# Optimization experiments

Hardware: AMD Instinct MI355X
Metric: run time of the kernel (lower is better)

Reference implementation:

```python
import jax, jax.numpy as jnp
import numpy as np

N_CLASS, N_SUPPORT, N_QUERY = 5, 5, 15
C, T, V = 128, 8, 25
LN_EPS = 1e-12


def setup_inputs() -> dict:
    key = jax.random.key(0)
    ks = jax.random.split(key, 6)
    n_tot = N_CLASS * (N_SUPPORT + N_QUERY)
    inp = jax.random.normal(ks[0], (n_tot, C, T, V), dtype=jnp.float32)
    # episode labels: 20 consecutive samples per class (arange // per_class)
    target = (jnp.arange(n_tot, dtype=jnp.int32) // (N_SUPPORT + N_QUERY)).astype(jnp.int32)
    s = 0.02
    p = lambda k: jax.random.normal(k, (C, C), dtype=jnp.float32) * s
    return {
        'input': inp,
        'Wq': p(ks[1]), 'bq': jnp.zeros((C,), jnp.float32),
        'Wk': p(ks[2]), 'bk': jnp.zeros((C,), jnp.float32),
        'Wv': p(ks[3]), 'bv': jnp.zeros((C,), jnp.float32),
        'Wo': p(ks[4]), 'bo': jnp.zeros((C,), jnp.float32),
        'ln_g': jnp.ones((C,), jnp.float32), 'ln_b': jnp.zeros((C,), jnp.float32),
        'target': target,
        'n_support': N_SUPPORT,
    }


def _layer_norm(x, g, b):
    mu = x.mean(-1, keepdims=True)
    var = ((x - mu) ** 2).mean(-1, keepdims=True)
    return (x - mu) * jax.lax.rsqrt(var + LN_EPS) * g + b


def _episode_forward(input, Wq, bq, Wk, bk, Wv, bv, Wo, bo, ln_g, ln_b, target, n_support):
    n_tot, c, t, v = input.shape
    m = N_CLASS
    per_class = n_tot // m
    n_query = per_class - n_support
    n = m * n_query

    # support/query split (stable argsort == torch.where per class for sorted labels)
    order = jnp.argsort(target).reshape(m, per_class)
    supp_idx = order[:, :n_support]                      # (m, h)
    qry_idx = order[:, n_support:].reshape(-1)           # (n,)
    z_proto = input[supp_idx]                            # (m, h, c, t, v)
    zq = input[qry_idx]                                  # (n, c, t, v)

    # ---- hal(): pairwise cross-attention over the vertex axis ----
    mh = m * n_support
    zq_p = jnp.transpose(zq, (0, 2, 3, 1))                                   # (n, t, v, c)
    zp_p = jnp.transpose(z_proto.reshape(mh, c, t, v), (0, 2, 3, 1))          # (mh, t, v, c)
    cat = jnp.concatenate([zq_p, zp_p], axis=0)                               # (n1, t, v, c)
    n1 = cat.shape[0]

    # Q from each of the n1 items, K/V from each of the mh prototypes.
    # Equivalent to the original expand->reshape pairing, without duplicating K/V.
    Q = cat @ Wq + bq                                                         # (n1, t, v, c)
    K = zp_p @ Wk + bk                                                        # (mh, t, v, c)
    Vv = zp_p @ Wv + bv                                                       # (mh, t, v, c)
    scale = 1.0 / jnp.sqrt(jnp.asarray(c, dtype=Q.dtype))
    scores = jnp.einsum('ntqc,mtkc->nmtqk', Q, K) * scale                     # (n1, mh, t, v, v)
    attn = jax.nn.softmax(scores, axis=-1)
    ctx = jnp.einsum('nmtqk,mtkc->nmtqc', attn, Vv)                           # (n1, mh, t, v, c)
    out = _layer_norm(ctx @ Wo + bo + cat[:, None], ln_g, ln_b)               # residual + LN
    att = out.mean(axis=1)                                                    # (n1, t, v, c) mean over mh pairs

    zq_att = jnp.transpose(att[:n], (0, 3, 1, 2))                             # (n, c, t, v)
    proto_att = att[n:].reshape(m, n_support, t, v, c).mean(axis=1)           # (m, t, v, c)
    proto_att = jnp.transpose(proto_att, (0, 3, 1, 2))                        # (m, c, t, v)

    # ---- squared-Euclidean metric on flattened features ----
    zq_f = zq_att.reshape(n, -1)
    zp_f = proto_att.reshape(m, -1)
    dist = jnp.sum((zq_f[:, None, :] - zp_f[None, :, :]) ** 2, axis=-1)       # (n, m)

    log_p_y = jax.nn.log_softmax(-dist, axis=1).reshape(m, n_query, m)
    cls = jnp.arange(m)
    loss = -log_p_y[cls[:, None], jnp.arange(n_query)[None, :], cls[:, None]].mean()
    y_hat = jnp.argmax(log_p_y, axis=2)
    acc = (y_hat == cls[:, None]).astype(jnp.float32).mean()
    return loss, acc


def reference(input, Wq, bq, Wk, bk, Wv, bv, Wo, bo, ln_g, ln_b, target, n_support):
    return _episode_forward(input, Wq, bq, Wk, bk, Wv, bv, Wo, bo, ln_g, ln_b, target, n_support)
```

## Files before the change

### kernel.cpp

```cpp
#include <hip/hip_runtime.h>
#include <math.h>

#define NTOT 100
#define NQ   75
#define NP   25
#define CC   128
#define TT   8
#define VV   25
#define NCLS 5
#define NSUP 5
#define NQRY 15
#define ROW  (TT*VV*CC)
#define TILE (VV*CC)
#define ROWS_Q 20000
#define ROWS_S 5000
#define RB_Q 625
#define RB_S 157

typedef __attribute__((ext_vector_type(8))) short short8;
typedef __attribute__((ext_vector_type(16))) float f32x16;

typedef union { uint4 u4; short8 s8; } pk_t;

__device__ __forceinline__ ushort f2bf(float f) {
    uint u = __float_as_uint(f);
    u += 0x7FFFu + ((u >> 16) & 1u);
    return (ushort)(u >> 16);
}
__device__ __forceinline__ float bf2f(uint u16v) {
    return __uint_as_float(u16v << 16);
}
__device__ __forceinline__ uint pkbf(float a, float b) {
    return (uint)f2bf(a) | ((uint)f2bf(b) << 16);
}

__global__ __launch_bounds__(256) void k_proj(
    const float* __restrict__ input, const int* __restrict__ target,
    const float* __restrict__ Wq, const float* __restrict__ Wk,
    const float* __restrict__ Wv, const float* __restrict__ Wo,
    const float* __restrict__ bq, const float* __restrict__ bk,
    const float* __restrict__ bv,
    ushort* __restrict__ catC, ushort* __restrict__ Qf,
    ushort* __restrict__ Kf, ushort* __restrict__ Vf,
    int* __restrict__ counter) {
    __shared__ ushort WfragLDS[16384];
    __shared__ ushort VtFrag[16384];

    int b = blockIdx.x, tid = threadIdx.x;
    int w = tid >> 6, lane = tid & 63, half = lane >> 5, l31 = lane & 31;

    if (b == 0 && tid == 0) *counter = 0;

    int* iscr = (int*)VtFrag;
    if (tid < NTOT) iscr[tid] = target[tid];
    __syncthreads();
    if (tid < NTOT) {
        int ti = iscr[tid], rank = 0;
        for (int j = 0; j < NTOT; ++j) {
            int tj = iscr[j];
            rank += (tj < ti) || (tj == ti && j < tid);
        }
        iscr[128 + rank] = tid;
    }
    __syncthreads();

    bool isQ = b < 157;
    int rowblk = isQ ? (b * 4 + w) : ((b - 157) * 4 + w);
    int nrb = isQ ? RB_Q : RB_S;
    bool act = rowblk < nrb;
    int rlimit = isQ ? ROWS_Q : ROWS_S;
    int grow = rowblk * 32 + l31;
    int growc = grow < rlimit ? grow : rlimit - 1;
    int n = growc / 200;
    int tv = growc - n * 200;
    int src;
    {
        int nn = isQ ? n : (NQ + n);
        if (nn < NQ) { int m = nn / NQRY, qq = nn - m * NQRY; src = iscr[128 + m * 20 + NSUP + qq]; }
        else         { int i2 = nn - NQ; int m = i2 / NSUP, s = i2 - m * NSUP; src = iscr[128 + m * 20 + s]; }
    }
    __syncthreads();

    const float* inp = input + (size_t)src * ROW + tv;
    short8 af[8];
    #pragma unroll
    for (int ks = 0; ks < 8; ++ks) {
        float f0 = inp[(ks * 16 + half * 8 + 0) * 200];
        float f1 = inp[(ks * 16 + half * 8 + 1) * 200];
        float f2 = inp[(ks * 16 + half * 8 + 2) * 200];
        float f3 = inp[(ks * 16 + half * 8 + 3) * 200];
        float f4 = inp[(ks * 16 + half * 8 + 4) * 200];
        float f5 = inp[(ks * 16 + half * 8 + 5) * 200];
        float f6 = inp[(ks * 16 + half * 8 + 6) * 200];
        float f7 = inp[(ks * 16 + half * 8 + 7) * 200];
        pk_t u;
        u.u4 = make_uint4(pkbf(f0, f1), pkbf(f2, f3), pkbf(f4, f5), pkbf(f6, f7));
        af[ks] = u.s8;
    }

    #define BUILDW(W) do {                                                       \
        for (int o = tid; o < 2048; o += 256) {                                  \
            int k8 = o >> 7, c = o & 127;                                        \
            uint4 pk;                                                            \
            pk.x = pkbf((W)[(k8*8+0)*128 + c], (W)[(k8*8+1)*128 + c]);           \
            pk.y = pkbf((W)[(k8*8+2)*128 + c], (W)[(k8*8+3)*128 + c]);           \
            pk.z = pkbf((W)[(k8*8+4)*128 + c], (W)[(k8*8+5)*128 + c]);           \
            pk.w = pkbf((W)[(k8*8+6)*128 + c], (W)[(k8*8+7)*128 + c]);           \
            int dst = (((c >> 5) * 8 + (k8 >> 1)) * 64 + ((c & 31) + 32 * (k8 & 1))) * 8; \
            *(uint4*)(WfragLDS + dst) = pk;                                      \
        }                                                                        \
    } while (0)

    if (isQ) {
        BUILDW(Wq);
        __syncthreads();
        #pragma unroll
        for (int ct = 0; ct < 4; ++ct) {
            if (!act) continue;
            f32x16 Cm;
            #pragma unroll
            for (int r = 0; r < 16; ++r) Cm[r] = 0.f;
            const ushort* bp = WfragLDS + ct * 8 * 512 + lane * 8;
            #pragma unroll
            for (int ks = 0; ks < 8; ++ks) {
                short8 bf_ = *(const short8*)(bp + ks * 512);
                Cm = __builtin_amdgcn_mfma_f32_32x32x16_bf16(af[ks], bf_, Cm, 0, 0, 0);
            }
            float bcol = bq[ct * 32 + l31];
            #pragma unroll
            for (int r = 0; r < 16; ++r) {
                int row = rowblk * 32 + (r & 3) + 8 * (r >> 2) + 4 * half;
                if (row < ROWS_Q) {
                    int c = ct * 32 + l31;
                    int st = row / 25, vv = row - st * 25;
                    size_t dst = (((size_t)st * 8 + (c >> 4)) * 64 + (vv + 32 * ((c >> 3) & 1))) * 8 + (c & 7);
                    Qf[dst] = f2bf(Cm[r] + bcol);
                }
            }
        }
        if (act) {
            ushort* cc = catC + (size_t)grow * 128 + half * 8;
            #pragma unroll
            for (int ks = 0; ks < 8; ++ks)
                *(short8*)(cc + ks * 16) = af[ks];
        }
    } else {
        BUILDW(Wk);
        __syncthreads();
        #pragma unroll
        for (int ct = 0; ct < 4; ++ct) {
            if (!act) continue;
            f32x16 Cm;
            #pragma unroll
            for (int r = 0; r < 16; ++r) Cm[r] = 0.f;
            const ushort* bp = WfragLDS + ct * 8 * 512 + lane * 8;
            #pragma unroll
            for (int ks = 0; ks < 8; ++ks) {
                short8 bf_ = *(const short8*)(bp + ks * 512);
                Cm = __builtin_amdgcn_mfma_f32_32x32x16_bf16(af[ks], bf_, Cm, 0, 0, 0);
            }
            float bcol = bk[ct * 32 + l31];
            #pragma unroll
            for (int r = 0; r < 16; ++r) {
                int row = rowblk * 32 + (r & 3) + 8 * (r >> 2) + 4 * half;
                if (row < ROWS_S) {
                    int c = ct * 32 + l31;
                    int st = row / 25, vv = row - st * 25;
                    size_t dst = (((size_t)st * 8 + (c >> 4)) * 64 + (vv + 32 * ((c >> 3) & 1))) * 8 + (c & 7);
                    Kf[dst] = f2bf(Cm[r] + bcol);
                }
            }
        }
        __syncthreads();
        BUILDW(Wv);
        __syncthreads();
        #pragma unroll
        for (int ct = 0; ct < 4; ++ct) {
            if (!act) continue;
            f32x16 Cm;
            #pragma unroll
            for (int r = 0; r < 16; ++r) Cm[r] = 0.f;
            const ushort* bp = WfragLDS + ct * 8 * 512 + lane * 8;
            #pragma unroll
            for (int ks = 0; ks < 8; ++ks) {
                short8 bf_ = *(const short8*)(bp + ks * 512);
                Cm = __builtin_amdgcn_mfma_f32_32x32x16_bf16(af[ks], bf_, Cm, 0, 0, 0);
            }
            float bcol = bv[ct * 32 + l31];
            int c = ct * 32 + l31;
            int ks2 = c >> 4, lh = (c >> 3) & 1, j2 = c & 7;
            #pragma unroll
            for (int r = 0; r < 16; ++r) {
                int rowLocal = (r & 3) + 8 * (r >> 2) + 4 * half;
                VtFrag[w * 4096 + ks2 * 512 + (rowLocal + 32 * lh) * 8 + j2] = f2bf(Cm[r] + bcol);
            }
        }
        __syncthreads();
        BUILDW(Wo);
        __syncthreads();
        short8 a2[8];
        if (act) {
            #pragma unroll
            for (int ks = 0; ks < 8; ++ks)
                a2[ks] = *(const short8*)(VtFrag + w * 4096 + ks * 512 + lane * 8);
        }
        #pragma unroll
        for (int ct = 0; ct < 4; ++ct) {
            if (!act) continue;
            f32x16 Cm;
            #pragma unroll
            for (int r = 0; r < 16; ++r) Cm[r] = 0.f;
            const ushort* bp = WfragLDS + ct * 8 * 512 + lane * 8;
            #pragma unroll
            for (int ks = 0; ks < 8; ++ks) {
                short8 bf_ = *(const short8*)(bp + ks * 512);
                Cm = __builtin_amdgcn_mfma_f32_32x32x16_bf16(a2[ks], bf_, Cm, 0, 0, 0);
            }
            #pragma unroll
            for (int r = 0; r < 16; ++r) {
                int row = rowblk * 32 + (r & 3) + 8 * (r >> 2) + 4 * half;
                if (row < ROWS_S) {
                    int c = ct * 32 + l31;
                    int tile = row / 25, vv = row - tile * 25;
                    size_t dst = ((((size_t)tile * 4 + ct) * 2 + (vv >> 4)) * 64
                                  + ((c & 31) + 32 * ((vv & 15) >> 3))) * 8 + (vv & 7);
                    Vf[dst] = f2bf(Cm[r]);
                }
            }
        }
    }
    #undef BUILDW
}

__global__ __launch_bounds__(256, 2) void k_attn(
    const ushort* __restrict__ Qf, const ushort* __restrict__ Kf,
    const ushort* __restrict__ Vf, const ushort* __restrict__ catC,
    const float* __restrict__ bo, float* __restrict__ att) {
    __shared__ float catb[25 * 129];
    __shared__ float red[2][50][65];
    __shared__ ushort qls[4096];

    int pair = blockIdx.x;
    int t = pair & 7;
    int tid = threadIdx.x;
    int wv = tid >> 6, lane = tid & 63;
    int q = lane & 31, half = lane >> 5;

    {
        const uint* cc = (const uint*)catC + (size_t)pair * 1600;
        for (int i2 = tid; i2 < 1600; i2 += 256) {
            uint u = cc[i2];
            int r = i2 >> 6, c2 = (i2 & 63) * 2;
            catb[r * 129 + c2]     = bf2f(u & 0xffffu) + bo[c2];
            catb[r * 129 + c2 + 1] = bf2f(u >> 16) + bo[c2 + 1];
        }
    }
    {
        const uint* qp = (const uint*)(Qf + (size_t)pair * 4096);
        uint* ql = (uint*)qls;
        for (int i2 = tid; i2 < 2048; i2 += 256) ql[i2] = qp[i2];
    }
    __syncthreads();

    int qc = q < 25 ? q : 24;
    float attsum[64];
    #pragma unroll
    for (int i = 0; i < 64; ++i) attsum[i] = 0.f;
    float Csc = 0.f;

    const float CEXP = (float)(1.4426950408889634 * 0.08838834764831845);

    const ushort* kbase = Kf + (size_t)t * 4096 + lane * 8;
    short8 kf[8];
    #pragma unroll
    for (int ks = 0; ks < 8; ++ks)
        kf[ks] = *(const short8*)(kbase + (size_t)wv * 32768 + ks * 512);

    int cnt = (wv == 0) ? 7 : 6;
    for (int mi = 0; mi < cnt; ++mi) {
        int m = wv + 4 * mi;

        f32x16 S;
        #pragma unroll
        for (int r = 0; r < 16; ++r) S[r] = 0.f;
        #pragma unroll
        for (int ks = 0; ks < 8; ++ks) {
            short8 qv = *(const short8*)(qls + ks * 512 + lane * 8);
            S = __builtin_amdgcn_mfma_f32_32x32x16_bf16(kf[ks], qv, S, 0, 0, 0);
        }

        float p[16], mx = -3e38f;
        #pragma unroll
        for (int r = 0; r < 16; ++r) {
            int key = (r & 3) + 8 * (r >> 2) + 4 * half;
            float v = (key < 25) ? S[r] : -3e38f;
            p[r] = v; mx = fmaxf(mx, v);
        }
        mx = fmaxf(mx, __shfl_xor(mx, 32));
        float sum = 0.f;
        #pragma unroll
        for (int r = 0; r < 16; ++r) { p[r] = exp2f((p[r] - mx) * CEXP); sum += p[r]; }
        sum += __shfl_xor(sum, 32);
        float inv = 1.f / sum;

        const ushort* vp = Vf + ((size_t)(m * 8 + t)) * 4096 + lane * 8;
        short8 vf0 = *(const short8*)(vp);
        short8 vf1 = *(const short8*)(vp + 512);
        short8 vf2 = *(const short8*)(vp + 1024);
        short8 vf3 = *(const short8*)(vp + 1536);
        short8 vf4 = *(const short8*)(vp + 2048);
        short8 vf5 = *(const short8*)(vp + 2560);
        short8 vf6 = *(const short8*)(vp + 3072);
        short8 vf7 = *(const short8*)(vp + 3584);
        #pragma unroll
        for (int ks = 0; ks < 8; ++ks)
            kf[ks] = *(const short8*)(kbase + (size_t)(m + 4) * 32768 + ks * 512);

        uint o01   = pkbf(p[0] * inv,  p[1] * inv);
        uint o23   = pkbf(p[2] * inv,  p[3] * inv);
        uint o45   = pkbf(p[4] * inv,  p[5] * inv);
        uint o67   = pkbf(p[6] * inv,  p[7] * inv);
        uint o89   = pkbf(p[8] * inv,  p[9] * inv);
        uint o1011 = pkbf(p[10] * inv, p[11] * inv);
        uint o1213 = pkbf(p[12] * inv, p[13] * inv);
        uint o1415 = pkbf(p[14] * inv, p[15] * inv);
        bool h0 = (half == 0);
        uint rA = __shfl_xor(h0 ? o45 : o01, 32);
        uint rB = __shfl_xor(h0 ? o67 : o23, 32);
        uint rC = __shfl_xor(h0 ? o1213 : o89, 32);
        uint rD = __shfl_xor(h0 ? o1415 : o1011, 32);
        pk_t P0, P1;
        P0.u4 = h0 ? make_uint4(o01, o23, rA, rB) : make_uint4(rA, rB, o45, o67);
        P1.u4 = h0 ? make_uint4(o89, o1011, rC, rD) : make_uint4(rC, rD, o1213, o1415);
        short8 pb0 = P0.s8, pb1 = P1.s8;

        f32x16 ctx[4];
        #pragma unroll
        for (int mt = 0; mt < 4; ++mt) {
            #pragma unroll
            for (int r = 0; r < 16; ++r) ctx[mt][r] = 0.f;
        }
        ctx[0] = __builtin_amdgcn_mfma_f32_32x32x16_bf16(vf0, pb0, ctx[0], 0, 0, 0);
        ctx[0] = __builtin_amdgcn_mfma_f32_32x32x16_bf16(vf1, pb1, ctx[0], 0, 0, 0);
        ctx[1] = __builtin_amdgcn_mfma_f32_32x32x16_bf16(vf2, pb0, ctx[1], 0, 0, 0);
        ctx[1] = __builtin_amdgcn_mfma_f32_32x32x16_bf16(vf3, pb1, ctx[1], 0, 0, 0);
        ctx[2] = __builtin_amdgcn_mfma_f32_32x32x16_bf16(vf4, pb0, ctx[2], 0, 0, 0);
        ctx[2] = __builtin_amdgcn_mfma_f32_32x32x16_bf16(vf5, pb1, ctx[2], 0, 0, 0);
        ctx[3] = __builtin_amdgcn_mfma_f32_32x32x16_bf16(vf6, pb0, ctx[3], 0, 0, 0);
        ctx[3] = __builtin_amdgcn_mfma_f32_32x32x16_bf16(vf7, pb1, ctx[3], 0, 0, 0);

        float s1 = 0.f, s2 = 0.f;
        #pragma unroll
        for (int mt = 0; mt < 4; ++mt) {
            float t1 = 0.f, t2 = 0.f;
            #pragma unroll
            for (int r = 0; r < 16; ++r) {
                int c = mt * 32 + (r & 3) + 8 * (r >> 2) + 4 * half;
                float xv = ctx[mt][r] + catb[qc * 129 + c];
                ctx[mt][r] = xv;
                t1 += xv; t2 = fmaf(xv, xv, t2);
            }
            s1 += t1; s2 += t2;
        }
        s1 += __shfl_xor(s1, 32); s2 += __shfl_xor(s2, 32);
        float mu = s1 * (1.f / 128.f);
        float var = s2 * (1.f / 128.f) - mu * mu;
        var = fmaxf(var, 0.f);
        float rs = rsqrtf(var + 1e-12f);
        #pragma unroll
        for (int i = 0; i < 64; ++i)
            attsum[i] = fmaf(ctx[i >> 4][i & 15], rs, attsum[i]);
        Csc = fmaf(-mu, rs, Csc);
    }

    __syncthreads();
    int s = half * 25 + q;
    bool act = q < 25;
    if ((wv == 1 || wv == 3) && act) {
        float (*rg)[65] = red[wv >> 1];
        #pragma unroll
        for (int i = 0; i < 64; ++i) rg[s][i] = attsum[i];
        rg[s][64] = Csc;
    }
    __syncthreads();
    if ((wv == 0 || wv == 2) && act) {
        float (*rg)[65] = red[wv >> 1];
        #pragma unroll
        for (int i = 0; i < 64; ++i) attsum[i] += rg[s][i];
        Csc += rg[s][64];
    }
    __syncthreads();
    if (wv == 2 && act) {
        #pragma unroll
        for (int i = 0; i < 64; ++i) red[0][s][i] = attsum[i];
        red[0][s][64] = Csc;
    }
    __syncthreads();
    if (wv == 0 && act) {
        #pragma unroll
        for (int i = 0; i < 64; ++i) attsum[i] += red[0][s][i];
        Csc += red[0][s][64];
        float* ap = att + (size_t)pair * TILE + q * 128;
        #pragma unroll
        for (int mt = 0; mt < 4; ++mt) {
            #pragma unroll
            for (int rg4 = 0; rg4 < 4; ++rg4) {
                int c0 = mt * 32 + 8 * rg4 + 4 * half;
                int i0 = mt * 16 + rg4 * 4;
                float4 o;
                o.x = attsum[i0 + 0] + Csc; o.y = attsum[i0 + 1] + Csc;
                o.z = attsum[i0 + 2] + Csc; o.w = attsum[i0 + 3] + Csc;
                *(float4*)&ap[c0] = o;
            }
        }
    }
}

__global__ __launch_bounds__(256) void k_dist_loss(
    const float* __restrict__ att, const float* __restrict__ ln_g,
    float* __restrict__ dist, int* __restrict__ counter,
    float* __restrict__ out) {
    int b = blockIdx.x;
    int i = b / 5, j = b - 5 * i;
    const float4* a  = (const float4*)(att + (size_t)i * ROW);
    const float4* s0 = (const float4*)(att + (size_t)(NQ + j * 5 + 0) * ROW);
    const float4* s1p = (const float4*)(att + (size_t)(NQ + j * 5 + 1) * ROW);
    const float4* s2p = (const float4*)(att + (size_t)(NQ + j * 5 + 2) * ROW);
    const float4* s3p = (const float4*)(att + (size_t)(NQ + j * 5 + 3) * ROW);
    const float4* s4p = (const float4*)(att + (size_t)(NQ + j * 5 + 4) * ROW);
    float d = 0.f;
    for (int e4 = threadIdx.x; e4 < 6400; e4 += 256) {
        float4 av = a[e4];
        float4 q0 = s0[e4], q1 = s1p[e4], q2 = s2p[e4], q3 = s3p[e4], q4 = s4p[e4];
        float4 g4 = *(const float4*)(ln_g + (e4 & 31) * 4);
        float px = 0.2f * (q0.x + q1.x + q2.x + q3.x + q4.x);
        float py = 0.2f * (q0.y + q1.y + q2.y + q3.y + q4.y);
        float pz = 0.2f * (q0.z + q1.z + q2.z + q3.z + q4.z);
        float pw = 0.2f * (q0.w + q1.w + q2.w + q3.w + q4.w);
        float dx = av.x - px, dy = av.y - py, dz = av.z - pz, dw = av.w - pw;
        d = fmaf(g4.x * g4.x, dx * dx, d);
        d = fmaf(g4.y * g4.y, dy * dy, d);
        d = fmaf(g4.z * g4.z, dz * dz, d);
        d = fmaf(g4.w * g4.w, dw * dw, d);
    }
    #pragma unroll
    for (int msk = 32; msk >= 1; msk >>= 1) d += __shfl_xor(d, msk);
    __shared__ float part[4];
    __shared__ int lastFlag;
    int lane = threadIdx.x & 63, wv = threadIdx.x >> 6;
    if (lane == 0) part[wv] = d;
    __syncthreads();
    if (threadIdx.x == 0) {
        float total = (part[0] + part[1] + part[2] + part[3]) * (1.f / 625.f);
        __hip_atomic_store(&dist[b], total, __ATOMIC_RELEASE, __HIP_MEMORY_SCOPE_AGENT);
        int tk = __hip_atomic_fetch_add(counter, 1, __ATOMIC_ACQ_REL, __HIP_MEMORY_SCOPE_AGENT);
        lastFlag = (tk == 374);
    }
    __syncthreads();
    if (!lastFlag) return;

    int iq = threadIdx.x;
    float li = 0.f, ok = 0.f;
    if (iq < NQ) {
        float dd[5];
        #pragma unroll
        for (int jj = 0; jj < 5; ++jj)
            dd[jj] = __hip_atomic_load(&dist[iq * 5 + jj], __ATOMIC_ACQUIRE, __HIP_MEMORY_SCOPE_AGENT);
        int cls = iq / NQRY;
        float mind = dd[0];
        int best = 0;
        #pragma unroll
        for (int jj = 1; jj < 5; ++jj) {
            if (dd[jj] < mind) mind = dd[jj];
            if (dd[jj] < dd[best]) best = jj;
        }
        float sume = 0.f;
        #pragma unroll
        for (int jj = 0; jj < 5; ++jj) sume += expf(mind - dd[jj]);
        float lse = logf(sume) - mind;
        li = dd[cls] + lse;
        ok = (best == cls) ? 1.f : 0.f;
    }
    #pragma unroll
    for (int msk = 32; msk >= 1; msk >>= 1) {
        li += __shfl_xor(li, msk);
        ok += __shfl_xor(ok, msk);
    }
    if (lane == 0) { part[wv] = li; part[wv + 2] = ok; }
    __syncthreads();
    if (threadIdx.x == 0) {
        out[0] = (part[0] + part[1]) / 75.f;
        out[1] = (part[2] + part[3]) / 75.f;
    }
}

extern "C" void kernel_launch(void* const* d_in, const int* in_sizes, int n_in,
                              void* d_out, int out_size, void* d_ws, size_t ws_size,
                              hipStream_t stream) {
    const float* input = (const float*)d_in[0];
    const float* Wq   = (const float*)d_in[1];
    const float* bq   = (const float*)d_in[2];
    const float* Wk   = (const float*)d_in[3];
    const float* bk   = (const float*)d_in[4];
    const float* Wv   = (const float*)d_in[5];
    const float* bv   = (const float*)d_in[6];
    const float* Wo   = (const float*)d_in[7];
    const float* bo   = (const float*)d_in[8];
    const float* ln_g = (const float*)d_in[9];
    const float* ln_b = (const float*)d_in[10];
    const int* target = (const int*)d_in[11];
    float* out = (float*)d_out;
    (void)ln_b;

    float* ws = (float*)d_ws;
    ushort* catC = (ushort*)ws;
    ushort* Qf   = catC + 2560000;
    ushort* Kf   = Qf + 3276800;
    ushort* Vf   = Kf + 819200;
    float*  att  = (float*)(Vf + 819200);
    float*  distb = att + 2560000;
    int*    counter = (int*)(distb + 512);

    k_proj<<<197, 256, 0, stream>>>(input, target, Wq, Wk, Wv, Wo, bq, bk, bv,
                                    catC, Qf, Kf, Vf, counter);
    k_attn<<<800, 256, 0, stream>>>(Qf, Kf, Vf, catC, bo, att);
    k_dist_loss<<<375, 256, 0, stream>>>(att, ln_g, distb, counter, out);
}
```

Baseline: 187.1 us.

## Split projection work so each block owns one row tile and waves split columns

The projection kernel now launches one block per 32-row tile (782 blocks instead of 197). Each wave computes one 32-column slice of the output instead of every wave computing all four slices for its own row tile. Input rows are staged through LDS with c-major loads that are contiguous along the tv axis, and catC is written from that staging buffer. This raises parallelism and makes the input reads coalesced. In exchange, every block rebuilds the bf16 weight fragments, which adds redundant weight reads and conversion work.

```diff
diff --git a/kernel.cpp b/kernel.cpp
--- a/kernel.cpp
+++ b/kernel.cpp
@@ -43,15 +43,16 @@
     ushort* __restrict__ catC, ushort* __restrict__ Qf,
     ushort* __restrict__ Kf, ushort* __restrict__ Vf,
     int* __restrict__ counter) {
-    __shared__ ushort WfragLDS[16384];
-    __shared__ ushort VtFrag[16384];
-
-    int b = blockIdx.x, tid = threadIdx.x;
+    __shared__ ushort stage[32 * 132];
+    __shared__ ushort Wf[16384];
+    __shared__ ushort VtF[4096];
+    __shared__ int iscr[200];
+
+    int bid = blockIdx.x, tid = threadIdx.x;
     int w = tid >> 6, lane = tid & 63, half = lane >> 5, l31 = lane & 31;
 
-    if (b == 0 && tid == 0) *counter = 0;
-
-    int* iscr = (int*)VtFrag;
+    if (bid == 0 && tid == 0) *counter = 0;
+
     if (tid < NTOT) iscr[tid] = target[tid];
     __syncthreads();
     if (tid < NTOT) {
@@ -60,42 +61,30 @@
             int tj = iscr[j];
             rank += (tj < ti) || (tj == ti && j < tid);
         }
-        iscr[128 + rank] = tid;
-    }
-    __syncthreads();
-
-    bool isQ = b < 157;
-    int rowblk = isQ ? (b * 4 + w) : ((b - 157) * 4 + w);
-    int nrb = isQ ? RB_Q : RB_S;
-    bool act = rowblk < nrb;
+        iscr[100 + rank] = tid;
+    }
+    __syncthreads();
+
+    bool isQ = bid < RB_Q;
+    int rowblk = isQ ? bid : bid - RB_Q;
     int rlimit = isQ ? ROWS_Q : ROWS_S;
-    int grow = rowblk * 32 + l31;
-    int growc = grow < rlimit ? grow : rlimit - 1;
-    int n = growc / 200;
-    int tv = growc - n * 200;
-    int src;
-    {
-        int nn = isQ ? n : (NQ + n);
-        if (nn < NQ) { int m = nn / NQRY, qq = nn - m * NQRY; src = iscr[128 + m * 20 + NSUP + qq]; }
-        else         { int i2 = nn - NQ; int m = i2 / NSUP, s = i2 - m * NSUP; src = iscr[128 + m * 20 + s]; }
-    }
-    __syncthreads();
-
-    const float* inp = input + (size_t)src * ROW + tv;
-    short8 af[8];
-    #pragma unroll
-    for (int ks = 0; ks < 8; ++ks) {
-        float f0 = inp[(ks * 16 + half * 8 + 0) * 200];
-        float f1 = inp[(ks * 16 + half * 8 + 1) * 200];
-        float f2 = inp[(ks * 16 + half * 8 + 2) * 200];
-        float f3 = inp[(ks * 16 + half * 8 + 3) * 200];
-        float f4 = inp[(ks * 16 + half * 8 + 4) * 200];
-        float f5 = inp[(ks * 16 + half * 8 + 5) * 200];
-        float f6 = inp[(ks * 16 + half * 8 + 6) * 200];
-        float f7 = inp[(ks * 16 + half * 8 + 7) * 200];
-        pk_t u;
-        u.u4 = make_uint4(pkbf(f0, f1), pkbf(f2, f3), pkbf(f4, f5), pkbf(f6, f7));
-        af[ks] = u.s8;
+    int g0 = rowblk * 32;
+    int gend = min(g0 + 32, rlimit);
+
+    for (int nn = g0 / 200; nn <= (gend - 1) / 200; ++nn) {
+        int lo = max(g0 - nn * 200, 0);
+        int hi = min(gend - 1 - nn * 200, 199);
+        int len = hi - lo + 1;
+        int nidx = isQ ? nn : (NQ + nn);
+        int src;
+        if (nidx < NQ) { int m = nidx / NQRY, qq = nidx - m * NQRY; src = iscr[100 + m * 20 + NSUP + qq]; }
+        else           { int i2 = nidx - NQ; int m = i2 / NSUP, s = i2 - m * NSUP; src = iscr[100 + m * 20 + s]; }
+        const float* inb = input + (size_t)src * ROW + lo;
+        int rbase = nn * 200 + lo - g0;
+        for (int idx = tid; idx < len * 128; idx += 256) {
+            int c = idx / len, k = idx - c * len;
+            stage[(rbase + k) * 132 + c] = f2bf(inb[c * 200 + k]);
+        }
     }
 
     #define BUILDW(W) do {                                                       \
@@ -107,64 +96,58 @@
             pk.z = pkbf((W)[(k8*8+4)*128 + c], (W)[(k8*8+5)*128 + c]);           \
             pk.w = pkbf((W)[(k8*8+6)*128 + c], (W)[(k8*8+7)*128 + c]);           \
             int dst = (((c >> 5) * 8 + (k8 >> 1)) * 64 + ((c & 31) + 32 * (k8 & 1))) * 8; \
-            *(uint4*)(WfragLDS + dst) = pk;                                      \
+            *(uint4*)(Wf + dst) = pk;                                            \
         }                                                                        \
     } while (0)
 
+    BUILDW(isQ ? Wq : Wk);
+    __syncthreads();
+
+    short8 af[8];
+    #pragma unroll
+    for (int ks = 0; ks < 8; ++ks)
+        af[ks] = *(const short8*)&stage[l31 * 132 + ks * 16 + half * 8];
+
+    #define CHAIN(A, OUT) do {                                                   \
+        const ushort* bp_ = Wf + w * 4096 + lane * 8;                            \
+        _Pragma("unroll")                                                        \
+        for (int ks = 0; ks < 8; ++ks) {                                         \
+            short8 bf_ = *(const short8*)(bp_ + ks * 512);                       \
+            OUT = __builtin_amdgcn_mfma_f32_32x32x16_bf16(A[ks], bf_, OUT, 0, 0, 0); \
+        }                                                                        \
+    } while (0)
+
     if (isQ) {
-        BUILDW(Wq);
-        __syncthreads();
-        #pragma unroll
-        for (int ct = 0; ct < 4; ++ct) {
-            if (!act) continue;
+        f32x16 Cm;
+        #pragma unroll
+        for (int r = 0; r < 16; ++r) Cm[r] = 0.f;
+        CHAIN(af, Cm);
+        float bcol = bq[w * 32 + l31];
+        int c = w * 32 + l31;
+        #pragma unroll
+        for (int r = 0; r < 16; ++r) {
+            int row = g0 + (r & 3) + 8 * (r >> 2) + 4 * half;
+            int st = row / 25, vv = row - st * 25;
+            size_t dst = (((size_t)st * 8 + (c >> 4)) * 64 + (vv + 32 * ((c >> 3) & 1))) * 8 + (c & 7);
+            Qf[dst] = f2bf(Cm[r] + bcol);
+        }
+        uint* cc = (uint*)catC + (size_t)g0 * 64;
+        for (int idx = tid; idx < 2048; idx += 256) {
+            int row = idx >> 6, c2 = (idx & 63) * 2;
+            cc[idx] = (uint)stage[row * 132 + c2] | ((uint)stage[row * 132 + c2 + 1] << 16);
+        }
+    } else {
+        {
             f32x16 Cm;
             #pragma unroll
             for (int r = 0; r < 16; ++r) Cm[r] = 0.f;
-            const ushort* bp = WfragLDS + ct * 8 * 512 + lane * 8;
-            #pragma unroll
-            for (int ks = 0; ks < 8; ++ks) {
-                short8 bf_ = *(const short8*)(bp + ks * 512);
-                Cm = __builtin_amdgcn_mfma_f32_32x32x16_bf16(af[ks], bf_, Cm, 0, 0, 0);
-            }
-            float bcol = bq[ct * 32 + l31];
+            CHAIN(af, Cm);
+            float bcol = bk[w * 32 + l31];
+            int c = w * 32 + l31;
             #pragma unroll
             for (int r = 0; r < 16; ++r) {
-                int row = rowblk * 32 + (r & 3) + 8 * (r >> 2) + 4 * half;
-                if (row < ROWS_Q) {
-                    int c = ct * 32 + l31;
-                    int st = row / 25, vv = row - st * 25;
-                    size_t dst = (((size_t)st * 8 + (c >> 4)) * 64 + (vv + 32 * ((c >> 3) & 1))) * 8 + (c & 7);
-                    Qf[dst] = f2bf(Cm[r] + bcol);
-                }
-            }
-        }
-        if (act) {
-            ushort* cc = catC + (size_t)grow * 128 + half * 8;
-            #pragma unroll
-            for (int ks = 0; ks < 8; ++ks)
-                *(short8*)(cc + ks * 16) = af[ks];
-        }
-    } else {
-        BUILDW(Wk);
-        __syncthreads();
-        #pragma unroll
-        for (int ct = 0; ct < 4; ++ct) {
-            if (!act) continue;
-            f32x16 Cm;
-            #pragma unroll
-            for (int r = 0; r < 16; ++r) Cm[r] = 0.f;
-            const ushort* bp = WfragLDS + ct * 8 * 512 + lane * 8;
-            #pragma unroll
-            for (int ks = 0; ks < 8; ++ks) {
-                short8 bf_ = *(const short8*)(bp + ks * 512);
-                Cm = __builtin_amdgcn_mfma_f32_32x32x16_bf16(af[ks], bf_, Cm, 0, 0, 0);
-            }
-            float bcol = bk[ct * 32 + l31];
-            #pragma unroll
-            for (int r = 0; r < 16; ++r) {
-                int row = rowblk * 32 + (r & 3) + 8 * (r >> 2) + 4 * half;
+                int row = g0 + (r & 3) + 8 * (r >> 2) + 4 * half;
                 if (row < ROWS_S) {
-                    int c = ct * 32 + l31;
                     int st = row / 25, vv = row - st * 25;
                     size_t dst = (((size_t)st * 8 + (c >> 4)) * 64 + (vv + 32 * ((c >> 3) & 1))) * 8 + (c & 7);
                     Kf[dst] = f2bf(Cm[r] + bcol);
@@ -174,61 +157,46 @@
         __syncthreads();
         BUILDW(Wv);
         __syncthreads();
-        #pragma unroll
-        for (int ct = 0; ct < 4; ++ct) {
-            if (!act) continue;
+        {
             f32x16 Cm;
             #pragma unroll
             for (int r = 0; r < 16; ++r) Cm[r] = 0.f;
-            const ushort* bp = WfragLDS + ct * 8 * 512 + lane * 8;
-            #pragma unroll
-            for (int ks = 0; ks < 8; ++ks) {
-                short8 bf_ = *(const short8*)(bp + ks * 512);
-                Cm = __builtin_amdgcn_mfma_f32_32x32x16_bf16(af[ks], bf_, Cm, 0, 0, 0);
-            }
-            float bcol = bv[ct * 32 + l31];
-            int c = ct * 32 + l31;
-            int ks2 = c >> 4, lh = (c >> 3) & 1, j2 = c & 7;
+            CHAIN(af, Cm);
+            float bcol = bv[w * 32 + l31];
+            int c = w * 32 + l31;
+            int ks2 = c >> 4, kh = (c >> 3) & 1, j2 = c & 7;
             #pragma unroll
             for (int r = 0; r < 16; ++r) {
                 int rowLocal = (r & 3) + 8 * (r >> 2) + 4 * half;
-                VtFrag[w * 4096 + ks2 * 512 + (rowLocal + 32 * lh) * 8 + j2] = f2bf(Cm[r] + bcol);
+                VtF[ks2 * 512 + (rowLocal + 32 * kh) * 8 + j2] = f2bf(Cm[r] + bcol);
             }
         }
         __syncthreads();
         BUILDW(Wo);
         __syncthreads();
         short8 a2[8];
-        if (act) {
-            #pragma unroll
-            for (int ks = 0; ks < 8; ++ks)
-                a2[ks] = *(const short8*)(VtFrag + w * 4096 + ks * 512 + lane * 8);
-        }
-        #pragma unroll
-        for (int ct = 0; ct < 4; ++ct) {
-            if (!act) continue;
+        #pragma unroll
+        for (int ks = 0; ks < 8; ++ks)
+            a2[ks] = *(const short8*)&VtF[ks * 512 + lane * 8];
+        {
             f32x16 Cm;
             #pragma unroll
             for (int r = 0; r < 16; ++r) Cm[r] = 0.f;
-            const ushort* bp = WfragLDS + ct * 8 * 512 + lane * 8;
-            #pragma unroll
-            for (int ks = 0; ks < 8; ++ks) {
-                short8 bf_ = *(const short8*)(bp + ks * 512);
-                Cm = __builtin_amdgcn_mfma_f32_32x32x16_bf16(a2[ks], bf_, Cm, 0, 0, 0);
-            }
+            CHAIN(a2, Cm);
+            int c = w * 32 + l31;
             #pragma unroll
             for (int r = 0; r < 16; ++r) {
-                int row = rowblk * 32 + (r & 3) + 8 * (r >> 2) + 4 * half;
+                int row = g0 + (r & 3) + 8 * (r >> 2) + 4 * half;
                 if (row < ROWS_S) {
-                    int c = ct * 32 + l31;
                     int tile = row / 25, vv = row - tile * 25;
-                    size_t dst = ((((size_t)tile * 4 + ct) * 2 + (vv >> 4)) * 64
+                    size_t dst = ((((size_t)tile * 4 + (c >> 5)) * 2 + (vv >> 4)) * 64
                                   + ((c & 31) + 32 * ((vv & 15) >> 3))) * 8 + (vv & 7);
                     Vf[dst] = f2bf(Cm[r]);
                 }
             }
         }
     }
+    #undef CHAIN
     #undef BUILDW
 }
 
@@ -521,8 +489,8 @@
     float*  distb = att + 2560000;
     int*    counter = (int*)(distb + 512);
 
-    k_proj<<<197, 256, 0, stream>>>(input, target, Wq, Wk, Wv, Wo, bq, bk, bv,
-                                    catC, Qf, Kf, Vf, counter);
+    k_proj<<<RB_Q + RB_S, 256, 0, stream>>>(input, target, Wq, Wk, Wv, Wo, bq, bk, bv,
+                                            catC, Qf, Kf, Vf, counter);
     k_attn<<<800, 256, 0, stream>>>(Qf, Kf, Vf, catC, bo, att);
     k_dist_loss<<<375, 256, 0, stream>>>(att, ln_g, distb, counter, out);
 }
```

Result: no change. 183.9 us (-1.7%).
